# Kernel optimization log

Hardware: AMD Instinct MI355X
Metric: run time of the kernel (lower is better)

## Reference

```python
import jax, jax.numpy as jnp
import numpy as np

OFFSETS = (1, 2, 4, 8, 16, 64, 96, 192, 384, 512, 768, 1024)
J = 12
J_LARGE = 8  # offsets with index >= 4 use phase rotation


def _shift(x, d):
    """Return x shifted so out[..., n, :] = x[..., n-d, :]; zeros where n < d.
    Shift is along axis 2 (the sequence axis of [B,H,N,...])."""
    pad = [(0, 0)] * x.ndim
    pad[2] = (d, 0)
    return jnp.pad(x, pad)[:, :, : x.shape[2]]


def setup_inputs() -> dict:
    key = jax.random.key(0)
    ks = jax.random.split(key, 9)
    B, H, N, HD = 2, 16, 4096, 64
    f = jnp.float32
    q = jax.random.normal(ks[0], (B, H, N, HD), f)
    k = jax.random.normal(ks[1], (B, H, N, HD), f)
    v = jax.random.normal(ks[2], (B, H, N, HD), f)
    pb = jax.random.normal(ks[3], (J, H), f) * 0.1          # per-offset per-head score bias
    se = jax.random.normal(ks[4], (J, HD), f) * 0.1         # per-offset score embedding
    phase_base = jax.random.normal(ks[5], (J_LARGE, H, 2), f) * 0.1
    phase_gain = jax.random.normal(ks[6], (J_LARGE, H, 2), f) * 0.1
    y_pre = jax.random.normal(ks[7], (B, H, N, 2), f)       # query-side phase features
    z_pre = jax.random.normal(ks[8], (B, H, N, 2), f)       # key-side phase features
    return dict(q=q, k=k, v=v, pb=pb, se=se, phase_base=phase_base,
                phase_gain=phase_gain, y_pre=y_pre, z_pre=z_pre)


def reference(q, k, v, pb, se, phase_base, phase_gain, y_pre, z_pre):
    B, H, N, HD = q.shape
    sc = 1.0 / float(np.sqrt(HD))
    n_idx = jnp.arange(N)

    # --- scores over the J fixed causal offsets: s_i[n] = (q_n . (k_{n-d} + se_i)) * sc + pb[i,h]
    scores = []
    for i, d in enumerate(OFFSETS):
        ks_ = _shift(k, d)  # key at n - d
        s = (jnp.einsum('bhnd,bhnd->bhn', q, ks_)
             + jnp.einsum('bhnd,d->bhn', q, se[i])) * sc
        s = s + pb[i][None, :, None]
        valid = (n_idx >= d)[None, None, :]
        scores.append(jnp.where(valid, s, -jnp.inf))
    scores = jnp.stack(scores, axis=-1)  # [B,H,N,J]

    lse = jax.nn.logsumexp(scores, axis=-1)            # [B,H,N]
    safe_lse = jnp.where(jnp.isfinite(lse), lse, 0.0)  # rows with no valid offset -> alpha = 0
    alpha = jnp.exp(scores - safe_lse[..., None])      # [B,H,N,J]; -inf scores give exactly 0

    # --- weighted sum of (phase-rotated) values
    out = jnp.zeros_like(q)
    for i, d in enumerate(OFFSETS):
        vs = _shift(v, d)  # value at n - d: [B,H,N,HD]
        if i >= 4:
            pi = i - 4
            zs = _shift(z_pre, d)  # key-side phase features at n - d: [B,H,N,2]
            # theta_p = base[pi,h,p] + gain[pi,h,p] * y_pre[n,p] * z_pre[n-d,p]
            theta = (phase_base[pi][None, :, None, :]
                     + phase_gain[pi][None, :, None, :] * y_pre * zs)  # [B,H,N,2]
            c, s_ = jnp.cos(theta), jnp.sin(theta)
            v0, v1, v2, v3 = vs[..., 0], vs[..., 1], vs[..., 2], vs[..., 3]
            rot = jnp.stack([c[..., 0] * v0 - s_[..., 0] * v1,
                             s_[..., 0] * v0 + c[..., 0] * v1,
                             c[..., 1] * v2 - s_[..., 1] * v3,
                             s_[..., 1] * v2 + c[..., 1] * v3], axis=-1)
            vs = jnp.concatenate([rot, vs[..., 4:]], axis=-1)
        out = out + alpha[..., i:i + 1] * vs
    return out
```

## Files before the change

### kernel.cpp

```cpp
#include <hip/hip_runtime.h>


namespace {

constexpr int J   = 12;
constexpr int B_  = 2;
constexpr int H_  = 16;
constexpr int N_  = 4096;
constexpr int HD_ = 64;
constexpr int OFFS[J] = {1, 2, 4, 8, 16, 64, 96, 192, 384, 512, 768, 1024};

__global__ __launch_bounds__(256) void dsqg_kernel(
    const float* __restrict__ q, const float* __restrict__ k,
    const float* __restrict__ v, const float* __restrict__ pb,
    const float* __restrict__ se, const float* __restrict__ phase_base,
    const float* __restrict__ phase_gain, const float* __restrict__ y_pre,
    const float* __restrict__ z_pre, float* __restrict__ out)
{
    const int raw = blockIdx.x;
    const int per = gridDim.x >> 3;
    const int wid = (raw & 7) * per + (raw >> 3);

    const int bh    = wid >> 8;
    const int chunk = wid & 255;
    const int h     = bh & (H_ - 1);

    const int lane = threadIdx.x & 63;
    const int wave = threadIdx.x >> 6;
    const int grp  = lane & 15;
    const int n    = chunk * 16 + wave * 4 + (lane >> 4);

    const size_t base4 = (size_t)bh * N_ * (HD_ / 4);
    const float4* q4 = (const float4*)q + base4;
    const float4* k4 = (const float4*)k + base4;
    const float4* v4 = (const float4*)v + base4;
    float4*       o4 = (float4*)out + base4;

    const float4 qr = q4[(size_t)n * 16 + grp];

    int m[J];
    bool ok[J];
#pragma unroll
    for (int i = 0; i < J; ++i) {
        ok[i] = (n >= OFFS[i]);
        m[i]  = ok[i] ? (n - OFFS[i]) : 0;
    }

    float2 zr[8];
    float2 yp = make_float2(0.f, 0.f);
    if (grp == 0) {
        yp = ((const float2*)y_pre)[(size_t)bh * N_ + n];
#pragma unroll
        for (int pi = 0; pi < 8; ++pi)
            zr[pi] = ((const float2*)z_pre)[(size_t)bh * N_ + m[pi + 4]];
    }

    float4 kr[J];
#pragma unroll
    for (int i = 0; i < J; ++i) kr[i] = k4[(size_t)m[i] * 16 + grp];

    float p[J];
#pragma unroll
    for (int i = 0; i < J; ++i) {
        const float4 seg = ((const float4*)se)[i * 16 + grp];
        float t = qr.x * seg.x + qr.y * seg.y + qr.z * seg.z + qr.w * seg.w;
        t = fmaf(qr.x, kr[i].x, t);
        t = fmaf(qr.y, kr[i].y, t);
        t = fmaf(qr.z, kr[i].z, t);
        p[i] = fmaf(qr.w, kr[i].w, t);
    }

    float4 vr[J];
#pragma unroll
    for (int i = 0; i < J; ++i) vr[i] = v4[(size_t)m[i] * 16 + grp];

#pragma unroll
    for (int stage = 1; stage <= 8; stage <<= 1) {
#pragma unroll
        for (int i = 0; i < J; ++i) p[i] += __shfl_xor(p[i], stage);
    }

    const float sc = 0.125f;
    float e[J];
    float sum = 0.f;
#pragma unroll
    for (int i = 0; i < J; ++i) {
        const float si = fmaf(p[i], sc, pb[i * H_ + h]);
        e[i] = ok[i] ? __expf(si) : 0.f;
        sum += e[i];
    }

    if (grp == 0) {
#pragma unroll
        for (int pi = 0; pi < 8; ++pi) {
            const int i = pi + 4;
            const float b0 = phase_base[(pi * H_ + h) * 2 + 0];
            const float b1 = phase_base[(pi * H_ + h) * 2 + 1];
            const float g0 = phase_gain[(pi * H_ + h) * 2 + 0];
            const float g1 = phase_gain[(pi * H_ + h) * 2 + 1];
            const float th0 = fmaf(g0, yp.x * zr[pi].x, b0);
            const float th1 = fmaf(g1, yp.y * zr[pi].y, b1);
            const float c0 = __cosf(th0), s0 = __sinf(th0);
            const float c1 = __cosf(th1), s1 = __sinf(th1);
            const float v0 = vr[i].x, v1 = vr[i].y, v2 = vr[i].z, v3 = vr[i].w;
            vr[i].x = c0 * v0 - s0 * v1;
            vr[i].y = s0 * v0 + c0 * v1;
            vr[i].z = c1 * v2 - s1 * v3;
            vr[i].w = s1 * v2 + c1 * v3;
        }
    }

    float4 acc = make_float4(0.f, 0.f, 0.f, 0.f);
#pragma unroll
    for (int i = 0; i < J; ++i) {
        acc.x = fmaf(e[i], vr[i].x, acc.x);
        acc.y = fmaf(e[i], vr[i].y, acc.y);
        acc.z = fmaf(e[i], vr[i].z, acc.z);
        acc.w = fmaf(e[i], vr[i].w, acc.w);
    }

    float4 res;
    if (n >= 1) {
        const float inv = 1.0f / sum;
        res = make_float4(acc.x * inv, acc.y * inv, acc.z * inv, acc.w * inv);
    } else {
        res = make_float4(0.f, 0.f, 0.f, 0.f);
    }
    o4[(size_t)n * 16 + grp] = res;
}

}

extern "C" void kernel_launch(void* const* d_in, const int* in_sizes, int n_in,
                              void* d_out, int out_size, void* d_ws, size_t ws_size,
                              hipStream_t stream) {
    const float* q          = (const float*)d_in[0];
    const float* k          = (const float*)d_in[1];
    const float* v          = (const float*)d_in[2];
    const float* pb         = (const float*)d_in[3];
    const float* se         = (const float*)d_in[4];
    const float* phase_base = (const float*)d_in[5];
    const float* phase_gain = (const float*)d_in[6];
    const float* y_pre      = (const float*)d_in[7];
    const float* z_pre      = (const float*)d_in[8];
    float* out              = (float*)d_out;

    const int positions = B_ * H_ * N_;
    const int blocks    = positions / 16;
    dsqg_kernel<<<blocks, 256, 0, stream>>>(q, k, v, pb, se, phase_base,
                                            phase_gain, y_pre, z_pre, out);
}
```

Before: 190.1 us.

## Stream K/V chunks through LDS per 256-position tile with DPP reductions

New measurement: 283.2 us. 1.49x slower.

```diff
diff --git a/kernel.cpp b/kernel.cpp
--- a/kernel.cpp
+++ b/kernel.cpp
@@ -3,130 +3,209 @@
 
 namespace {
 
-constexpr int J   = 12;
-constexpr int B_  = 2;
-constexpr int H_  = 16;
-constexpr int N_  = 4096;
-constexpr int HD_ = 64;
+constexpr int J  = 12;
+constexpr int B_ = 2, H_ = 16, N_ = 4096;
+constexpr int T_ = 256;
+constexpr int C_ = 64;
 constexpr int OFFS[J] = {1, 2, 4, 8, 16, 64, 96, 192, 384, 512, 768, 1024};
 
-__global__ __launch_bounds__(256) void dsqg_kernel(
+template <int CTRL>
+__device__ __forceinline__ float dpp_add(float x) {
+    int t = __builtin_amdgcn_update_dpp(0, __float_as_int(x), CTRL, 0xf, 0xf, true);
+    return x + __int_as_float(t);
+}
+__device__ __forceinline__ float row16_reduce(float x) {
+    x = dpp_add<0xB1>(x);
+    x = dpp_add<0x4E>(x);
+    x = dpp_add<0x141>(x);
+    x = dpp_add<0x140>(x);
+    return x;
+}
+
+typedef const __attribute__((address_space(1))) void* gas_p;
+typedef __attribute__((address_space(3))) void*       las_p;
+
+__device__ __forceinline__ void gl_lds16(const float* g, float* l) {
+    __builtin_amdgcn_global_load_lds((gas_p)g, (las_p)l, 16, 0, 0);
+}
+__device__ __forceinline__ void gl_lds4(const float* g, float* l) {
+    __builtin_amdgcn_global_load_lds((gas_p)g, (las_p)l, 4, 0, 0);
+}
+
+__global__ __launch_bounds__(1024, 4) void dsqg_kernel(
     const float* __restrict__ q, const float* __restrict__ k,
     const float* __restrict__ v, const float* __restrict__ pb,
     const float* __restrict__ se, const float* __restrict__ phase_base,
     const float* __restrict__ phase_gain, const float* __restrict__ y_pre,
     const float* __restrict__ z_pre, float* __restrict__ out)
 {
+    __shared__ float  kvbuf[2][C_ * 64];
+    __shared__ float  sc_l[T_][J];
+    __shared__ float  zxy[2][2][C_];
+    __shared__ float2 ph_l[2][8];
+
     const int raw = blockIdx.x;
-    const int per = gridDim.x >> 3;
-    const int wid = (raw & 7) * per + (raw >> 3);
-
-    const int bh    = wid >> 8;
-    const int chunk = wid & 255;
-    const int h     = bh & (H_ - 1);
-
-    const int lane = threadIdx.x & 63;
-    const int wave = threadIdx.x >> 6;
-    const int grp  = lane & 15;
-    const int n    = chunk * 16 + wave * 4 + (lane >> 4);
-
-    const size_t base4 = (size_t)bh * N_ * (HD_ / 4);
+    const int wid = (raw & 7) * 64 + (raw >> 3);
+    const int bh  = wid >> 4;
+    const int n0  = (wid & 15) << 8;
+    const int h   = bh & (H_ - 1);
+
+    const int tid   = threadIdx.x;
+    const int lane  = tid & 63;
+    const int wv    = tid >> 6;
+    const int grp   = lane & 15;
+    const int g     = tid >> 4;
+    const int nbase = n0 + 4 * g;
+
+    const size_t base4 = (size_t)bh * N_ * 16;
     const float4* q4 = (const float4*)q + base4;
-    const float4* k4 = (const float4*)k + base4;
-    const float4* v4 = (const float4*)v + base4;
+    const float*  kf = k + (size_t)bh * N_ * 64;
+    const float*  vf = v + (size_t)bh * N_ * 64;
     float4*       o4 = (float4*)out + base4;
-
-    const float4 qr = q4[(size_t)n * 16 + grp];
-
-    int m[J];
-    bool ok[J];
+    const size_t  bhN = (size_t)bh * N_;
+    const float2* y2 = (const float2*)y_pre;
+    const float2* z2 = (const float2*)z_pre;
+
+    float4 qr[4];
+    float2 yv[4];
+#pragma unroll
+    for (int s = 0; s < 4; ++s) {
+        qr[s] = q4[(size_t)(nbase + s) * 16 + grp];
+        yv[s] = y2[bhN + nbase + s];
+    }
+    if (tid < 8) {
+        ph_l[0][tid] = ((const float2*)phase_base)[tid * H_ + h];
+        ph_l[1][tid] = ((const float2*)phase_gain)[tid * H_ + h];
+    }
+    float qse[4] = {0.f, 0.f, 0.f, 0.f};
 #pragma unroll
     for (int i = 0; i < J; ++i) {
-        ok[i] = (n >= OFFS[i]);
-        m[i]  = ok[i] ? (n - OFFS[i]) : 0;
-    }
-
-    float2 zr[8];
-    float2 yp = make_float2(0.f, 0.f);
-    if (grp == 0) {
-        yp = ((const float2*)y_pre)[(size_t)bh * N_ + n];
-#pragma unroll
-        for (int pi = 0; pi < 8; ++pi)
-            zr[pi] = ((const float2*)z_pre)[(size_t)bh * N_ + m[pi + 4]];
-    }
-
-    float4 kr[J];
-#pragma unroll
-    for (int i = 0; i < J; ++i) kr[i] = k4[(size_t)m[i] * 16 + grp];
-
-    float p[J];
-#pragma unroll
-    for (int i = 0; i < J; ++i) {
-        const float4 seg = ((const float4*)se)[i * 16 + grp];
-        float t = qr.x * seg.x + qr.y * seg.y + qr.z * seg.z + qr.w * seg.w;
-        t = fmaf(qr.x, kr[i].x, t);
-        t = fmaf(qr.y, kr[i].y, t);
-        t = fmaf(qr.z, kr[i].z, t);
-        p[i] = fmaf(qr.w, kr[i].w, t);
-    }
-
-    float4 vr[J];
-#pragma unroll
-    for (int i = 0; i < J; ++i) vr[i] = v4[(size_t)m[i] * 16 + grp];
-
-#pragma unroll
-    for (int stage = 1; stage <= 8; stage <<= 1) {
-#pragma unroll
-        for (int i = 0; i < J; ++i) p[i] += __shfl_xor(p[i], stage);
-    }
-
-    const float sc = 0.125f;
-    float e[J];
-    float sum = 0.f;
-#pragma unroll
-    for (int i = 0; i < J; ++i) {
-        const float si = fmaf(p[i], sc, pb[i * H_ + h]);
-        e[i] = ok[i] ? __expf(si) : 0.f;
-        sum += e[i];
-    }
-
-    if (grp == 0) {
-#pragma unroll
-        for (int pi = 0; pi < 8; ++pi) {
-            const int i = pi + 4;
-            const float b0 = phase_base[(pi * H_ + h) * 2 + 0];
-            const float b1 = phase_base[(pi * H_ + h) * 2 + 1];
-            const float g0 = phase_gain[(pi * H_ + h) * 2 + 0];
-            const float g1 = phase_gain[(pi * H_ + h) * 2 + 1];
-            const float th0 = fmaf(g0, yp.x * zr[pi].x, b0);
-            const float th1 = fmaf(g1, yp.y * zr[pi].y, b1);
-            const float c0 = __cosf(th0), s0 = __sinf(th0);
-            const float c1 = __cosf(th1), s1 = __sinf(th1);
-            const float v0 = vr[i].x, v1 = vr[i].y, v2 = vr[i].z, v3 = vr[i].w;
-            vr[i].x = c0 * v0 - s0 * v1;
-            vr[i].y = s0 * v0 + c0 * v1;
-            vr[i].z = c1 * v2 - s1 * v3;
-            vr[i].w = s1 * v2 + c1 * v3;
-        }
-    }
-
-    float4 acc = make_float4(0.f, 0.f, 0.f, 0.f);
-#pragma unroll
-    for (int i = 0; i < J; ++i) {
-        acc.x = fmaf(e[i], vr[i].x, acc.x);
-        acc.y = fmaf(e[i], vr[i].y, acc.y);
-        acc.z = fmaf(e[i], vr[i].z, acc.z);
-        acc.w = fmaf(e[i], vr[i].w, acc.w);
-    }
-
-    float4 res;
-    if (n >= 1) {
-        const float inv = 1.0f / sum;
-        res = make_float4(acc.x * inv, acc.y * inv, acc.z * inv, acc.w * inv);
-    } else {
-        res = make_float4(0.f, 0.f, 0.f, 0.f);
-    }
-    o4[(size_t)n * 16 + grp] = res;
+        const float4 sei = ((const float4*)se)[i * 16 + grp];
+#pragma unroll
+        for (int s = 0; s < 4; ++s) {
+            float t = qr[s].x * sei.x + qr[s].y * sei.y
+                    + qr[s].z * sei.z + qr[s].w * sei.w;
+            t = row16_reduce(t);
+            if (grp == i) qse[s] = t;
+        }
+    }
+
+    const int c_start = (n0 >= 1024) ? (n0 - 1024) : 0;
+    const int NC = (n0 + T_ - c_start) >> 6;
+
+    gl_lds16(kf + (size_t)(c_start + 4 * wv) * 64 + lane * 4,
+             &kvbuf[0][wv * 256 + lane * 4]);
+    for (int ci = 0; ci < NC; ++ci) {
+        __syncthreads();
+        if (ci + 1 < NC) {
+            const int c2 = c_start + (ci + 1) * C_;
+            gl_lds16(kf + (size_t)(c2 + 4 * wv) * 64 + lane * 4,
+                     &kvbuf[(ci + 1) & 1][wv * 256 + lane * 4]);
+        }
+        const int c = c_start + ci * C_;
+        const float* kb = kvbuf[ci & 1];
+#pragma unroll
+        for (int i = 0; i < J; ++i) {
+            const int base = c + OFFS[i];
+            if (base + C_ > n0 && base < n0 + T_) {
+#pragma unroll
+                for (int s = 0; s < 4; ++s) {
+                    const int n = nbase + s;
+                    if (n >= base && n < base + C_) {
+                        const int row = n - base;
+                        const float4 kr = *(const float4*)&kb[row * 64 + grp * 4];
+                        float t = qr[s].x * kr.x + qr[s].y * kr.y
+                                + qr[s].z * kr.z + qr[s].w * kr.w;
+                        t = row16_reduce(t);
+                        if (grp == i) sc_l[n - n0][i] = t + qse[s];
+                    }
+                }
+            }
+        }
+    }
+
+    gl_lds16(vf + (size_t)(c_start + 4 * wv) * 64 + lane * 4,
+             &kvbuf[0][wv * 256 + lane * 4]);
+    if (wv == 0) {
+        gl_lds4((const float*)(z2 + bhN + c_start) + lane * 2,     &zxy[0][0][lane]);
+        gl_lds4((const float*)(z2 + bhN + c_start) + lane * 2 + 1, &zxy[0][1][lane]);
+    }
+    __syncthreads();
+
+    if (tid < T_) {
+        const int n = n0 + tid;
+        float e[J];
+        float sum = 0.f;
+#pragma unroll
+        for (int i = 0; i < J; ++i) {
+            const float sv = sc_l[tid][i] * 0.125f + pb[i * H_ + h];
+            const float ev = (n >= OFFS[i]) ? __expf(sv) : 0.f;
+            e[i] = ev;
+            sum += ev;
+        }
+        const float inv = (sum > 0.f) ? (1.f / sum) : 0.f;
+#pragma unroll
+        for (int i = 0; i < J; ++i) sc_l[tid][i] = e[i] * inv;
+    }
+
+    float4 acc[4];
+#pragma unroll
+    for (int s = 0; s < 4; ++s) acc[s] = make_float4(0.f, 0.f, 0.f, 0.f);
+
+    for (int ci = 0; ci < NC; ++ci) {
+        __syncthreads();
+        if (ci + 1 < NC) {
+            const int c2 = c_start + (ci + 1) * C_;
+            const int b2 = (ci + 1) & 1;
+            gl_lds16(vf + (size_t)(c2 + 4 * wv) * 64 + lane * 4,
+                     &kvbuf[b2][wv * 256 + lane * 4]);
+            if (wv == 0) {
+                gl_lds4((const float*)(z2 + bhN + c2) + lane * 2,     &zxy[b2][0][lane]);
+                gl_lds4((const float*)(z2 + bhN + c2) + lane * 2 + 1, &zxy[b2][1][lane]);
+            }
+        }
+        const int c = c_start + ci * C_;
+        const int bsel = ci & 1;
+        const float* vb = kvbuf[bsel];
+#pragma unroll
+        for (int i = 0; i < J; ++i) {
+            const int base = c + OFFS[i];
+            if (base + C_ > n0 && base < n0 + T_) {
+#pragma unroll
+                for (int s = 0; s < 4; ++s) {
+                    const int n = nbase + s;
+                    if (n >= base && n < base + C_) {
+                        const int row = n - base;
+                        float4 vr = *(const float4*)&vb[row * 64 + grp * 4];
+                        const float w = sc_l[n - n0][i];
+                        if (i >= 4) {
+                            if (grp == 0) {
+                                const float zx = zxy[bsel][0][row];
+                                const float zy = zxy[bsel][1][row];
+                                const float th0 = fmaf(ph_l[1][i - 4].x, yv[s].x * zx, ph_l[0][i - 4].x);
+                                const float th1 = fmaf(ph_l[1][i - 4].y, yv[s].y * zy, ph_l[0][i - 4].y);
+                                const float c0 = __cosf(th0), s0 = __sinf(th0);
+                                const float c1 = __cosf(th1), s1 = __sinf(th1);
+                                const float a = vr.x, b = vr.y, cc = vr.z, dd = vr.w;
+                                vr.x = c0 * a - s0 * b;
+                                vr.y = s0 * a + c0 * b;
+                                vr.z = c1 * cc - s1 * dd;
+                                vr.w = s1 * cc + c1 * dd;
+                            }
+                        }
+                        acc[s].x = fmaf(w, vr.x, acc[s].x);
+                        acc[s].y = fmaf(w, vr.y, acc[s].y);
+                        acc[s].z = fmaf(w, vr.z, acc[s].z);
+                        acc[s].w = fmaf(w, vr.w, acc[s].w);
+                    }
+                }
+            }
+        }
+    }
+
+#pragma unroll
+    for (int s = 0; s < 4; ++s)
+        o4[(size_t)(nbase + s) * 16 + grp] = acc[s];
 }
 
 }
@@ -146,7 +225,7 @@
     float* out              = (float*)d_out;
 
     const int positions = B_ * H_ * N_;
-    const int blocks    = positions / 16;
-    dsqg_kernel<<<blocks, 256, 0, stream>>>(q, k, v, pb, se, phase_base,
-                                            phase_gain, y_pre, z_pre, out);
-}
+    const int blocks    = positions / T_;
+    dsqg_kernel<<<blocks, 1024, 0, stream>>>(q, k, v, pb, se, phase_base,
+                                             phase_gain, y_pre, z_pre, out);
+}
```
